# Optimization experiments

Measured on AMD Instinct MI355X. Metric: run time of the kernel, lower is better.

## Reference

```python
import jax, jax.numpy as jnp
import numpy as np

B, S, HID = 2, 2048, 1024
H, D = 16, HID // 16  # heads, head_dim
ROPE_BASE = 10000.0


def setup_inputs() -> dict:
    key = jax.random.key(0)
    k1, k2, k3, k4 = jax.random.split(key, 4)
    scale = 1.0 / np.sqrt(HID)
    return {
        "hidden_states": jax.random.normal(k1, (B, S, HID), dtype=jnp.float32),
        "attention_mask": jnp.zeros((B, 1, 1, S), dtype=jnp.float32),
        "Wq": jax.random.normal(k2, (HID, HID), dtype=jnp.float32) * scale,
        "Wk": jax.random.normal(k3, (HID, HID), dtype=jnp.float32) * scale,
        "Wv": jax.random.normal(k4, (HID, HID), dtype=jnp.float32) * scale,
    }


def _rope_cos_sin(seq_len, dim, dtype):
    inv_freq = 1.0 / (ROPE_BASE ** (jnp.arange(0, dim, 2, dtype=jnp.float32) / dim))
    freqs = jnp.arange(seq_len, dtype=jnp.float32)[:, None] * inv_freq[None, :]  # (S, D/2)
    emb = jnp.concatenate([freqs, freqs], axis=-1)  # (S, D)
    return jnp.cos(emb).astype(dtype), jnp.sin(emb).astype(dtype)


def _rotate_half(x):
    x1, x2 = jnp.split(x, 2, axis=-1)
    return jnp.concatenate([-x2, x1], axis=-1)


def reference(hidden_states, attention_mask, Wq, Wk, Wv):
    b, s, _ = hidden_states.shape
    # QKV projections (no bias), split into heads: (b, H, s, D)
    def proj(W):
        return jnp.einsum('bse,de->bsd', hidden_states, W).reshape(b, s, H, D).transpose(0, 2, 1, 3)
    q, k, v = proj(Wq), proj(Wk), proj(Wv)
    # Rotary embedding on q, k over sequence positions
    cos, sin = _rope_cos_sin(s, D, hidden_states.dtype)  # (s, D)
    cos = cos[None, None]  # (1,1,s,D)
    sin = sin[None, None]
    q = q * cos + _rotate_half(q) * sin
    k = k * cos + _rotate_half(k) * sin
    # Scaled dot-product attention with additive mask
    scores = jnp.einsum('bhqd,bhkd->bhqk', q, k) / jnp.sqrt(jnp.asarray(D, hidden_states.dtype))
    scores = scores + attention_mask
    probs = jax.nn.softmax(scores, axis=-1)  # dropout p=0 (eval) -> identity
    ctx = jnp.einsum('bhqk,bhkd->bhqd', probs, v)
    return ctx.transpose(0, 2, 1, 3).reshape(b, s, H * D)
```

## Files before the change

kernel.cpp:

```cpp
#include <hip/hip_runtime.h>
#include <stdint.h>

typedef unsigned short u16;
typedef short bf16x8 __attribute__((ext_vector_type(8)));
typedef float f32x4 __attribute__((ext_vector_type(4)));

#define S_ 2048
#define HID_ 1024
#define H_ 16
#define D_ 64

#define LOG2E 1.4426950408889634f
#define SCALE_LOG2 0.18033688011112042f
#define MAXC_LOG2 11.541560327111707f

__device__ __forceinline__ u16 f2bf(float f) {
  uint32_t x = __builtin_bit_cast(uint32_t, f);
  uint32_t r = (x + 0x7fffu + ((x >> 16) & 1u)) >> 16;
  return (u16)r;
}
__device__ __forceinline__ uint32_t packbf2(float a, float b) {
  return (uint32_t)f2bf(a) | ((uint32_t)f2bf(b) << 16);
}
__device__ __forceinline__ uint32_t permpack(float a, float b) {
  return __builtin_amdgcn_perm(__builtin_bit_cast(uint32_t, b),
                               __builtin_bit_cast(uint32_t, a), 0x07060302u);
}

__device__ __forceinline__ void gl2lds16(const void* g, void* l) {
  __builtin_amdgcn_global_load_lds(
      (const __attribute__((address_space(1))) unsigned int*)g,
      (__attribute__((address_space(3))) unsigned int*)l, 16, 0, 0);
}

#define NX_ (1 << 20)
#define NW_ (1 << 18)
#define NROPE_ 65536
__global__ void prep_kernel(const float* __restrict__ X, const float* __restrict__ Wq,
                            const float* __restrict__ Wk, const float* __restrict__ Wv,
                            const float* __restrict__ mask, u16* __restrict__ Xb,
                            u16* __restrict__ Wqb, u16* __restrict__ Wkb,
                            u16* __restrict__ Wvb, float* __restrict__ cos_t,
                            float* __restrict__ sin_t, float* __restrict__ mask2) {
  int i = blockIdx.x * 256 + threadIdx.x;
  if (i < NX_ + 3 * NW_) {
    const float* src;
    u16* dst;
    int off;
    if (i < NX_) {
      src = X; dst = Xb; off = i;
    } else if (i < NX_ + NW_) {
      src = Wq; dst = Wqb; off = i - NX_;
    } else if (i < NX_ + 2 * NW_) {
      src = Wk; dst = Wkb; off = i - NX_ - NW_;
    } else {
      src = Wv; dst = Wvb; off = i - NX_ - 2 * NW_;
    }
    float4 v = ((const float4*)src)[off];
    uint2 packed;
    packed.x = packbf2(v.x, v.y);
    packed.y = packbf2(v.z, v.w);
    ((uint2*)dst)[off] = packed;
  } else if (i < NX_ + 3 * NW_ + NROPE_) {
    int t = i - (NX_ + 3 * NW_);
    int s = t >> 5, j = t & 31;
    float invf = powf(10000.0f, -(float)j * (1.0f / 32.0f));
    float ang = (float)s * invf;
    cos_t[t] = cosf(ang);
    sin_t[t] = sinf(ang);
  } else {
    int t = i - (NX_ + 3 * NW_ + NROPE_);
    mask2[t] = fmaf(mask[t], LOG2E, -MAXC_LOG2);
  }
}

__global__ __launch_bounds__(512, 2) void qkv_gemm_kernel(
    const u16* __restrict__ X, const u16* __restrict__ Wq, const u16* __restrict__ Wk,
    const u16* __restrict__ Wv, const float* __restrict__ cos_t,
    const float* __restrict__ sin_t, u16* __restrict__ Q, u16* __restrict__ K,
    u16* __restrict__ Vt) {
  __shared__ char smem[131072];
  int tid = threadIdx.x;
  int lane = tid & 63, wave = tid >> 6;
  int wm = wave >> 2, wn = wave & 3;
  int quad = lane >> 4, l16 = lane & 15;
  int nbase = blockIdx.x * 128;
  int mbase = blockIdx.y * 128;

#define STAGE_ALL(k0, buf)                                                        \
  {                                                                               \
    _Pragma("unroll") for (int it = 0; it < 8; ++it) {                            \
      int j = (it & 1) * 512 + tid;                                               \
      int r = j >> 3, gs = j & 7, gsrc = gs ^ (r & 7);                            \
      const u16* src; int rb;                                                     \
      if ((it >> 1) == 0)      { src = X;  rb = mbase + r; }                      \
      else if ((it >> 1) == 1) { src = Wq; rb = nbase + r; }                      \
      else if ((it >> 1) == 2) { src = Wk; rb = nbase + r; }                      \
      else                     { src = Wv; rb = nbase + r; }                      \
      gl2lds16(src + (size_t)rb * HID_ + (k0) + gsrc * 8,                         \
               (buf) + (it >> 1) * 16384 + j * 16);                               \
    }                                                                             \
  }

  STAGE_ALL(0, smem)

  f32x4 acc[3][4][2] = {};

  for (int kk = 0; kk < 16; ++kk) {
    const char* buf = smem + (kk & 1) * 65536;
    __syncthreads();

    if (kk < 15)
      STAGE_ALL((kk + 1) * 64, smem + ((kk + 1) & 1) * 65536)

#pragma unroll
    for (int kh = 0; kh < 2; ++kh) {
      bf16x8 afrag[4];
#pragma unroll
      for (int i4 = 0; i4 < 4; ++i4) {
        int r = wm * 64 + i4 * 16 + l16;
        int L = r * 8 + ((kh * 4 + quad) ^ (r & 7));
        afrag[i4] = *(const bf16x8*)(buf + L * 16);
      }
#pragma unroll
      for (int w = 0; w < 3; ++w) {
        const char* Bs = buf + 16384 + w * 16384;
        bf16x8 bfrag[2];
#pragma unroll
        for (int j2 = 0; j2 < 2; ++j2) {
          int r = (wn >> 1) * 64 + (wn & 1) * 16 + j2 * 32 + l16;
          int L = r * 8 + ((kh * 4 + quad) ^ (r & 7));
          bfrag[j2] = *(const bf16x8*)(Bs + L * 16);
        }
        if (w == 2) {
#pragma unroll
          for (int i4 = 0; i4 < 4; ++i4)
#pragma unroll
            for (int j2 = 0; j2 < 2; ++j2)
              acc[2][i4][j2] = __builtin_amdgcn_mfma_f32_16x16x32_bf16(
                  afrag[i4], bfrag[j2], acc[2][i4][j2], 0, 0, 0);
        } else if (w == 1) {
#pragma unroll
          for (int i4 = 0; i4 < 4; ++i4)
#pragma unroll
            for (int j2 = 0; j2 < 2; ++j2)
              acc[1][i4][j2] = __builtin_amdgcn_mfma_f32_16x16x32_bf16(
                  bfrag[j2], afrag[i4], acc[1][i4][j2], 0, 0, 0);
        } else {
#pragma unroll
          for (int i4 = 0; i4 < 4; ++i4)
#pragma unroll
            for (int j2 = 0; j2 < 2; ++j2)
              acc[0][i4][j2] = __builtin_amdgcn_mfma_f32_16x16x32_bf16(
                  bfrag[j2], afrag[i4], acc[0][i4][j2], 0, 0, 0);
        }
      }
    }
  }
#undef STAGE_ALL

#pragma unroll
  for (int i4 = 0; i4 < 4; ++i4)
#pragma unroll
    for (int j2 = 0; j2 < 2; ++j2) {
      int m = mbase + wm * 64 + i4 * 16 + quad * 4;
      int n = nbase + (wn >> 1) * 64 + (wn & 1) * 16 + j2 * 32 + l16;
      int b = m >> 11, s0 = m & 2047;
      int h = n >> 6, d = n & 63;
      uint2 pk;
      pk.x = packbf2(acc[2][i4][j2][0], acc[2][i4][j2][1]);
      pk.y = packbf2(acc[2][i4][j2][2], acc[2][i4][j2][3]);
      *(uint2*)(Vt + (((size_t)(b * H_ + h)) * D_ + d) * S_ + s0) = pk;
    }

#pragma unroll
  for (int w = 0; w < 2; ++w) {
    u16* dst = (w == 0) ? Q : K;
#pragma unroll
    for (int i4 = 0; i4 < 4; ++i4) {
      int m = mbase + wm * 64 + i4 * 16 + l16;
      int n1 = nbase + (wn >> 1) * 64 + (wn & 1) * 16 + quad * 4;
      int b = m >> 11, s = m & 2047;
      int h = n1 >> 6, d1 = n1 & 63;
      float4 c4 = *(const float4*)(cos_t + s * 32 + d1);
      float4 s4 = *(const float4*)(sin_t + s * 32 + d1);
      float y1[4], y2[4];
#pragma unroll
      for (int r = 0; r < 4; ++r) {
        float cr = ((const float*)&c4)[r], sr = ((const float*)&s4)[r];
        float x1 = acc[w][i4][0][r], x2 = acc[w][i4][1][r];
        y1[r] = x1 * cr - x2 * sr;
        y2[r] = x2 * cr + x1 * sr;
      }
      size_t base = ((size_t)(b * H_ + h) * S_ + s) * D_;
      uint2 p1, p2;
      p1.x = packbf2(y1[0], y1[1]);
      p1.y = packbf2(y1[2], y1[3]);
      p2.x = packbf2(y2[0], y2[1]);
      p2.y = packbf2(y2[2], y2[3]);
      *(uint2*)(dst + base + d1) = p1;
      *(uint2*)(dst + base + d1 + 32) = p2;
    }
  }
}

__device__ __forceinline__ void pv_step(const bf16x8 (*pp)[2], const char* Vp, int quad,
                                        int l16, const bf16x8& ones, f32x4 (*o)[4],
                                        f32x4* lacc) {
  lacc[0] = __builtin_amdgcn_mfma_f32_16x16x32_bf16(pp[0][0], ones, lacc[0], 0, 0, 0);
  lacc[0] = __builtin_amdgcn_mfma_f32_16x16x32_bf16(pp[0][1], ones, lacc[0], 0, 0, 0);
  lacc[1] = __builtin_amdgcn_mfma_f32_16x16x32_bf16(pp[1][0], ones, lacc[1], 0, 0, 0);
  lacc[1] = __builtin_amdgcn_mfma_f32_16x16x32_bf16(pp[1][1], ones, lacc[1], 0, 0, 0);
#pragma unroll
  for (int jd = 0; jd < 4; ++jd) {
    int r = jd * 16 + l16;
#pragma unroll
    for (int kh = 0; kh < 2; ++kh) {
      int L = r * 8 + ((kh * 4 + quad) ^ (r & 7));
      bf16x8 vf = *(const bf16x8*)(Vp + L * 16);
      o[0][jd] = __builtin_amdgcn_mfma_f32_16x16x32_bf16(pp[0][kh], vf, o[0][jd], 0, 0, 0);
      o[1][jd] = __builtin_amdgcn_mfma_f32_16x16x32_bf16(pp[1][kh], vf, o[1][jd], 0, 0, 0);
    }
  }
}

__device__ __forceinline__ void qk_step(const char* Ks, const bf16x8 (*qfrag)[2], int quad,
                                        int l16, f32x4 (*s)[4]) {
#pragma unroll
  for (int jt = 0; jt < 4; ++jt) {
    int r = jt * 16 + l16;
#pragma unroll
    for (int kh = 0; kh < 2; ++kh) {
      int L = r * 8 + ((kh * 4 + quad) ^ (r & 7));
      bf16x8 kf = *(const bf16x8*)(Ks + L * 16);
      s[0][jt] = __builtin_amdgcn_mfma_f32_16x16x32_bf16(kf, qfrag[0][kh], s[0][jt], 0, 0, 0);
      s[1][jt] = __builtin_amdgcn_mfma_f32_16x16x32_bf16(kf, qfrag[1][kh], s[1][jt], 0, 0, 0);
    }
  }
}

__device__ __forceinline__ void softmax_pack(const f32x4 (*s)[4], const float4* mv,
                                             bf16x8 (*pp)[2]) {
#pragma unroll
  for (int qb = 0; qb < 2; ++qb) {
    uint32_t a[4][2];
#pragma unroll
    for (int jt = 0; jt < 4; ++jt) {
      float pf[4];
#pragma unroll
      for (int r = 0; r < 4; ++r) {
        float mvr = ((const float*)&mv[jt])[r];
        pf[r] = __builtin_amdgcn_exp2f(fmaf(s[qb][jt][r], SCALE_LOG2, mvr));
      }
      a[jt][0] = permpack(pf[0], pf[1]);
      a[jt][1] = permpack(pf[2], pf[3]);
    }
#pragma unroll
    for (int kh = 0; kh < 2; ++kh) {
      uint32_t tt[4];
#pragma unroll
      for (int i = 0; i < 2; ++i) {
        auto r1 = __builtin_amdgcn_permlane32_swap(a[2 * kh][i], a[2 * kh + 1][i],
                                                   false, false);
        auto r2 = __builtin_amdgcn_permlane16_swap(r1[0], r1[1], false, false);
        tt[i] = r2[0];
        tt[2 + i] = r2[1];
      }
      union { uint32_t u[4]; bf16x8 v; } cv;
      cv.u[0] = tt[0]; cv.u[1] = tt[1]; cv.u[2] = tt[2]; cv.u[3] = tt[3];
      pp[qb][kh] = cv.v;
    }
  }
}

__device__ __forceinline__ void stage_kv(const u16* Kbase, const u16* Vbase, char* Kn,
                                         int nb, int tid) {
#pragma unroll
  for (int half = 0; half < 2; ++half) {
    int i = half * 256 + tid;
    int r = i >> 3, gs = i & 7, gsrc = gs ^ (r & 7);
    gl2lds16(Kbase + (size_t)(nb + r) * D_ + gsrc * 8, Kn + i * 16);
    gl2lds16(Vbase + (size_t)r * S_ + nb + gsrc * 8, Kn + 8192 + i * 16);
  }
}

__global__ __launch_bounds__(256, 2) void flash_kernel(
    const u16* __restrict__ Q, const u16* __restrict__ K, const u16* __restrict__ Vt,
    const float* __restrict__ mask2, float* __restrict__ out) {
  __shared__ char smem[49152];
  int tid = threadIdx.x, wave = tid >> 6;
  int lane = tid & 63;
  int quad = lane >> 4, l16 = lane & 15;
  int bh = blockIdx.y, b = bh >> 4, h = bh & 15;
  int qbase = blockIdx.x * 128;
  int qw = qbase + wave * 32;
  const float* m2row = mask2 + b * S_;
  const u16* Kbase = K + (size_t)bh * S_ * D_;
  const u16* Vbase = Vt + (size_t)bh * D_ * S_;

  bf16x8 qfrag[2][2];
#pragma unroll
  for (int qb = 0; qb < 2; ++qb) {
    const u16* qp = Q + ((size_t)bh * S_ + qw + qb * 16 + l16) * D_ + quad * 8;
    qfrag[qb][0] = *(const bf16x8*)qp;
    qfrag[qb][1] = *(const bf16x8*)(qp + 32);
  }
  bf16x8 ones;
#pragma unroll
  for (int j = 0; j < 8; ++j) ones[j] = (short)0x3f80;

  f32x4 o[2][4] = {};
  f32x4 lacc[2] = {};
  bf16x8 pp[2][2];

  stage_kv(Kbase, Vbase, smem, 0, tid);
  float4 mv[4];
#pragma unroll
  for (int jt = 0; jt < 4; ++jt) mv[jt] = *(const float4*)(m2row + jt * 16 + quad * 4);

  {
    __syncthreads();
    stage_kv(Kbase, Vbase, smem + 16384, 64, tid);
    f32x4 s[2][4] = {};
    __builtin_amdgcn_s_setprio(1);
    qk_step(smem, qfrag, quad, l16, s);
    __builtin_amdgcn_s_setprio(0);
    softmax_pack(s, mv, pp);
#pragma unroll
    for (int jt = 0; jt < 4; ++jt)
      mv[jt] = *(const float4*)(m2row + 64 + jt * 16 + quad * 4);
  }

  for (int kt = 1; kt <= 30; ++kt) {
    char* Ks = smem + (kt % 3) * 16384;
    __syncthreads();
    stage_kv(Kbase, Vbase, smem + ((kt + 1) % 3) * 16384, (kt + 1) * 64, tid);

    __builtin_amdgcn_s_setprio(1);
    const char* Vp = smem + ((kt - 1) % 3) * 16384 + 8192;
    pv_step(pp, Vp, quad, l16, ones, o, lacc);

    f32x4 s[2][4] = {};
    qk_step(Ks, qfrag, quad, l16, s);
    __builtin_amdgcn_s_setprio(0);

    softmax_pack(s, mv, pp);
#pragma unroll
    for (int jt = 0; jt < 4; ++jt)
      mv[jt] = *(const float4*)(m2row + (kt + 1) * 64 + jt * 16 + quad * 4);
  }

  {
    __syncthreads();
    __builtin_amdgcn_s_setprio(1);
    pv_step(pp, smem + 0 * 16384 + 8192, quad, l16, ones, o, lacc);
    f32x4 s[2][4] = {};
    qk_step(smem + 16384, qfrag, quad, l16, s);
    __builtin_amdgcn_s_setprio(0);
    softmax_pack(s, mv, pp);
  }

  pv_step(pp, smem + 16384 + 8192, quad, l16, ones, o, lacc);

  float inv[2][4];
#pragma unroll
  for (int qb = 0; qb < 2; ++qb)
#pragma unroll
    for (int r = 0; r < 4; ++r) inv[qb][r] = 1.0f / lacc[qb][r];
#pragma unroll
  for (int qb = 0; qb < 2; ++qb)
#pragma unroll
    for (int jd = 0; jd < 4; ++jd) {
#pragma unroll
      for (int r = 0; r < 4; ++r) {
        int d = jd * 16 + l16;
        int q = qw + qb * 16 + quad * 4 + r;
        out[(((size_t)b * S_ + q) * H_ + h) * D_ + d] = o[qb][jd][r] * inv[qb][r];
      }
    }
}

extern "C" void kernel_launch(void* const* d_in, const int* in_sizes, int n_in,
                              void* d_out, int out_size, void* d_ws, size_t ws_size,
                              hipStream_t stream) {
  const float* hid = (const float*)d_in[0];
  const float* mask = (const float*)d_in[1];
  const float* Wq = (const float*)d_in[2];
  const float* Wk = (const float*)d_in[3];
  const float* Wv = (const float*)d_in[4];
  float* out = (float*)d_out;
  char* ws = (char*)d_ws;

  u16* Xbf = (u16*)ws;
  u16* Wqb = (u16*)(ws + (8u << 20));
  u16* Wkb = (u16*)(ws + (10u << 20));
  u16* Wvb = (u16*)(ws + (12u << 20));
  u16* Qb = (u16*)(ws + (14u << 20));
  u16* Kb = (u16*)(ws + (22u << 20));
  u16* Vtb = (u16*)(ws + (30u << 20));
  float* cos_t = (float*)(ws + (38u << 20));
  float* sin_t = (float*)(ws + (38u << 20) + (256u << 10));
  float* mask2 = (float*)(ws + (38u << 20) + (512u << 10));

  prep_kernel<<<7440, 256, 0, stream>>>(hid, Wq, Wk, Wv, mask, Xbf, Wqb, Wkb, Wvb,
                                        cos_t, sin_t, mask2);
  qkv_gemm_kernel<<<dim3(8, 32), 512, 0, stream>>>(Xbf, Wqb, Wkb, Wvb, cos_t, sin_t,
                                                   Qb, Kb, Vtb);
  flash_kernel<<<dim3(16, 32), 256, 0, stream>>>(Qb, Kb, Vtb, mask2, out);
}
```

Baseline: 160.2 us.

## Load K/V fragments directly from global into registers, dropping LDS staging

Removes the shared-memory triple-buffered K/V staging and its per-tile barriers. Each wave now loads its own K and V MFMA fragments straight from global memory into registers, prefetching the next tile after the current tile's MFMAs. This avoids LDS traffic and synchronisation, but each of the four waves re-reads the same K/V tile from global/L2 with no sharing across the block. It also leaves only about one stage of latency hiding.

```diff
diff --git a/kernel.cpp b/kernel.cpp
--- a/kernel.cpp
+++ b/kernel.cpp
@@ -204,41 +204,6 @@
   }
 }
 
-__device__ __forceinline__ void pv_step(const bf16x8 (*pp)[2], const char* Vp, int quad,
-                                        int l16, const bf16x8& ones, f32x4 (*o)[4],
-                                        f32x4* lacc) {
-  lacc[0] = __builtin_amdgcn_mfma_f32_16x16x32_bf16(pp[0][0], ones, lacc[0], 0, 0, 0);
-  lacc[0] = __builtin_amdgcn_mfma_f32_16x16x32_bf16(pp[0][1], ones, lacc[0], 0, 0, 0);
-  lacc[1] = __builtin_amdgcn_mfma_f32_16x16x32_bf16(pp[1][0], ones, lacc[1], 0, 0, 0);
-  lacc[1] = __builtin_amdgcn_mfma_f32_16x16x32_bf16(pp[1][1], ones, lacc[1], 0, 0, 0);
-#pragma unroll
-  for (int jd = 0; jd < 4; ++jd) {
-    int r = jd * 16 + l16;
-#pragma unroll
-    for (int kh = 0; kh < 2; ++kh) {
-      int L = r * 8 + ((kh * 4 + quad) ^ (r & 7));
-      bf16x8 vf = *(const bf16x8*)(Vp + L * 16);
-      o[0][jd] = __builtin_amdgcn_mfma_f32_16x16x32_bf16(pp[0][kh], vf, o[0][jd], 0, 0, 0);
-      o[1][jd] = __builtin_amdgcn_mfma_f32_16x16x32_bf16(pp[1][kh], vf, o[1][jd], 0, 0, 0);
-    }
-  }
-}
-
-__device__ __forceinline__ void qk_step(const char* Ks, const bf16x8 (*qfrag)[2], int quad,
-                                        int l16, f32x4 (*s)[4]) {
-#pragma unroll
-  for (int jt = 0; jt < 4; ++jt) {
-    int r = jt * 16 + l16;
-#pragma unroll
-    for (int kh = 0; kh < 2; ++kh) {
-      int L = r * 8 + ((kh * 4 + quad) ^ (r & 7));
-      bf16x8 kf = *(const bf16x8*)(Ks + L * 16);
-      s[0][jt] = __builtin_amdgcn_mfma_f32_16x16x32_bf16(kf, qfrag[0][kh], s[0][jt], 0, 0, 0);
-      s[1][jt] = __builtin_amdgcn_mfma_f32_16x16x32_bf16(kf, qfrag[1][kh], s[1][jt], 0, 0, 0);
-    }
-  }
-}
-
 __device__ __forceinline__ void softmax_pack(const f32x4 (*s)[4], const float4* mv,
                                              bf16x8 (*pp)[2]) {
 #pragma unroll
@@ -273,30 +238,17 @@
   }
 }
 
-__device__ __forceinline__ void stage_kv(const u16* Kbase, const u16* Vbase, char* Kn,
-                                         int nb, int tid) {
-#pragma unroll
-  for (int half = 0; half < 2; ++half) {
-    int i = half * 256 + tid;
-    int r = i >> 3, gs = i & 7, gsrc = gs ^ (r & 7);
-    gl2lds16(Kbase + (size_t)(nb + r) * D_ + gsrc * 8, Kn + i * 16);
-    gl2lds16(Vbase + (size_t)r * S_ + nb + gsrc * 8, Kn + 8192 + i * 16);
-  }
-}
-
 __global__ __launch_bounds__(256, 2) void flash_kernel(
     const u16* __restrict__ Q, const u16* __restrict__ K, const u16* __restrict__ Vt,
     const float* __restrict__ mask2, float* __restrict__ out) {
-  __shared__ char smem[49152];
   int tid = threadIdx.x, wave = tid >> 6;
   int lane = tid & 63;
   int quad = lane >> 4, l16 = lane & 15;
   int bh = blockIdx.y, b = bh >> 4, h = bh & 15;
-  int qbase = blockIdx.x * 128;
-  int qw = qbase + wave * 32;
+  int qw = blockIdx.x * 128 + wave * 32;
   const float* m2row = mask2 + b * S_;
-  const u16* Kbase = K + (size_t)bh * S_ * D_;
-  const u16* Vbase = Vt + (size_t)bh * D_ * S_;
+  const u16* kptr = K + (size_t)bh * S_ * D_ + (size_t)l16 * D_ + quad * 8;
+  const u16* vptr = Vt + (size_t)bh * D_ * S_ + (size_t)l16 * S_ + quad * 8;
 
   bf16x8 qfrag[2][2];
 #pragma unroll
@@ -311,56 +263,72 @@
 
   f32x4 o[2][4] = {};
   f32x4 lacc[2] = {};
-  bf16x8 pp[2][2];
-
-  stage_kv(Kbase, Vbase, smem, 0, tid);
+
+  bf16x8 kf[4][2], vf[4][2];
+#pragma unroll
+  for (int jt = 0; jt < 4; ++jt)
+#pragma unroll
+    for (int kh = 0; kh < 2; ++kh)
+      kf[jt][kh] = *(const bf16x8*)(kptr + (size_t)(jt * 16) * D_ + kh * 32);
+#pragma unroll
+  for (int jd = 0; jd < 4; ++jd)
+#pragma unroll
+    for (int kh = 0; kh < 2; ++kh)
+      vf[jd][kh] = *(const bf16x8*)(vptr + (size_t)(jd * 16) * S_ + kh * 32);
   float4 mv[4];
 #pragma unroll
   for (int jt = 0; jt < 4; ++jt) mv[jt] = *(const float4*)(m2row + jt * 16 + quad * 4);
 
-  {
-    __syncthreads();
-    stage_kv(Kbase, Vbase, smem + 16384, 64, tid);
+  for (int kt = 0; kt < 32; ++kt) {
+    int ktn = kt + (kt < 31);
+
     f32x4 s[2][4] = {};
     __builtin_amdgcn_s_setprio(1);
-    qk_step(smem, qfrag, quad, l16, s);
+#pragma unroll
+    for (int jt = 0; jt < 4; ++jt)
+#pragma unroll
+      for (int kh = 0; kh < 2; ++kh) {
+        s[0][jt] = __builtin_amdgcn_mfma_f32_16x16x32_bf16(kf[jt][kh], qfrag[0][kh],
+                                                           s[0][jt], 0, 0, 0);
+        s[1][jt] = __builtin_amdgcn_mfma_f32_16x16x32_bf16(kf[jt][kh], qfrag[1][kh],
+                                                           s[1][jt], 0, 0, 0);
+      }
     __builtin_amdgcn_s_setprio(0);
+
+#pragma unroll
+    for (int jt = 0; jt < 4; ++jt)
+#pragma unroll
+      for (int kh = 0; kh < 2; ++kh)
+        kf[jt][kh] = *(const bf16x8*)(kptr + ((size_t)ktn * 64 + jt * 16) * D_ + kh * 32);
+
+    bf16x8 pp[2][2];
     softmax_pack(s, mv, pp);
 #pragma unroll
     for (int jt = 0; jt < 4; ++jt)
-      mv[jt] = *(const float4*)(m2row + 64 + jt * 16 + quad * 4);
-  }
-
-  for (int kt = 1; kt <= 30; ++kt) {
-    char* Ks = smem + (kt % 3) * 16384;
-    __syncthreads();
-    stage_kv(Kbase, Vbase, smem + ((kt + 1) % 3) * 16384, (kt + 1) * 64, tid);
+      mv[jt] = *(const float4*)(m2row + ktn * 64 + jt * 16 + quad * 4);
 
     __builtin_amdgcn_s_setprio(1);
-    const char* Vp = smem + ((kt - 1) % 3) * 16384 + 8192;
-    pv_step(pp, Vp, quad, l16, ones, o, lacc);
-
-    f32x4 s[2][4] = {};
-    qk_step(Ks, qfrag, quad, l16, s);
+    lacc[0] = __builtin_amdgcn_mfma_f32_16x16x32_bf16(pp[0][0], ones, lacc[0], 0, 0, 0);
+    lacc[0] = __builtin_amdgcn_mfma_f32_16x16x32_bf16(pp[0][1], ones, lacc[0], 0, 0, 0);
+    lacc[1] = __builtin_amdgcn_mfma_f32_16x16x32_bf16(pp[1][0], ones, lacc[1], 0, 0, 0);
+    lacc[1] = __builtin_amdgcn_mfma_f32_16x16x32_bf16(pp[1][1], ones, lacc[1], 0, 0, 0);
+#pragma unroll
+    for (int jd = 0; jd < 4; ++jd)
+#pragma unroll
+      for (int kh = 0; kh < 2; ++kh) {
+        o[0][jd] = __builtin_amdgcn_mfma_f32_16x16x32_bf16(pp[0][kh], vf[jd][kh],
+                                                           o[0][jd], 0, 0, 0);
+        o[1][jd] = __builtin_amdgcn_mfma_f32_16x16x32_bf16(pp[1][kh], vf[jd][kh],
+                                                           o[1][jd], 0, 0, 0);
+      }
     __builtin_amdgcn_s_setprio(0);
 
-    softmax_pack(s, mv, pp);
-#pragma unroll
-    for (int jt = 0; jt < 4; ++jt)
-      mv[jt] = *(const float4*)(m2row + (kt + 1) * 64 + jt * 16 + quad * 4);
-  }
-
-  {
-    __syncthreads();
-    __builtin_amdgcn_s_setprio(1);
-    pv_step(pp, smem + 0 * 16384 + 8192, quad, l16, ones, o, lacc);
-    f32x4 s[2][4] = {};
-    qk_step(smem + 16384, qfrag, quad, l16, s);
-    __builtin_amdgcn_s_setprio(0);
-    softmax_pack(s, mv, pp);
-  }
-
-  pv_step(pp, smem + 16384 + 8192, quad, l16, ones, o, lacc);
+#pragma unroll
+    for (int jd = 0; jd < 4; ++jd)
+#pragma unroll
+      for (int kh = 0; kh < 2; ++kh)
+        vf[jd][kh] = *(const bf16x8*)(vptr + (size_t)(jd * 16) * S_ + ktn * 64 + kh * 32);
+  }
 
   float inv[2][4];
 #pragma unroll
```

Measured after the change: 236.6 us. +47.7%, slower.

## Deepen flash attention pipeline with separate K/V ring buffers and double score registers

Applied to the files above, without the earlier changes.

Restructures the attention main loop into a deeper software pipeline. K tiles now use a 2-slot ring and V tiles a 4-slot ring in LDS, and scores are held in two alternating register sets. In each iteration the loop issues PV for tile kt-2, QK for tile kt, and softmax for tile kt-1, so the exp/softmax work can overlap with the MFMA QK of the next tile. This costs more registers (an extra score set), which may pressure occupancy at 2 blocks/CU.

```diff
diff --git a/kernel.cpp b/kernel.cpp
--- a/kernel.cpp
+++ b/kernel.cpp
@@ -273,14 +273,14 @@
   }
 }
 
-__device__ __forceinline__ void stage_kv(const u16* Kbase, const u16* Vbase, char* Kn,
-                                         int nb, int tid) {
-#pragma unroll
-  for (int half = 0; half < 2; ++half) {
-    int i = half * 256 + tid;
+__device__ __forceinline__ void stage_kv2(const u16* Kbase, const u16* Vbase, char* Kd,
+                                          char* Vd, int nb, int tid) {
+#pragma unroll
+  for (int hh = 0; hh < 2; ++hh) {
+    int i = hh * 256 + tid;
     int r = i >> 3, gs = i & 7, gsrc = gs ^ (r & 7);
-    gl2lds16(Kbase + (size_t)(nb + r) * D_ + gsrc * 8, Kn + i * 16);
-    gl2lds16(Vbase + (size_t)r * S_ + nb + gsrc * 8, Kn + 8192 + i * 16);
+    gl2lds16(Kbase + (size_t)(nb + r) * D_ + gsrc * 8, Kd + i * 16);
+    gl2lds16(Vbase + (size_t)r * S_ + nb + gsrc * 8, Vd + i * 16);
   }
 }
 
@@ -292,8 +292,7 @@
   int lane = tid & 63;
   int quad = lane >> 4, l16 = lane & 15;
   int bh = blockIdx.y, b = bh >> 4, h = bh & 15;
-  int qbase = blockIdx.x * 128;
-  int qw = qbase + wave * 32;
+  int qw = blockIdx.x * 128 + wave * 32;
   const float* m2row = mask2 + b * S_;
   const u16* Kbase = K + (size_t)bh * S_ * D_;
   const u16* Vbase = Vt + (size_t)bh * D_ * S_;
@@ -311,56 +310,70 @@
 
   f32x4 o[2][4] = {};
   f32x4 lacc[2] = {};
+  f32x4 sA[2][4], sB[2][4];
   bf16x8 pp[2][2];
 
-  stage_kv(Kbase, Vbase, smem, 0, tid);
+#define ZERO_S(S)                                                 \
+  _Pragma("unroll") for (int qb = 0; qb < 2; ++qb)                \
+  _Pragma("unroll") for (int jt = 0; jt < 4; ++jt)                \
+      S[qb][jt] = (f32x4){0.f, 0.f, 0.f, 0.f};
+
+#define KSLOT(t) (smem + ((t) & 1) * 8192)
+#define VSLOT(t) (smem + 16384 + ((t) & 3) * 8192)
+
+  stage_kv2(Kbase, Vbase, KSLOT(0), VSLOT(0), 0, tid);
   float4 mv[4];
 #pragma unroll
   for (int jt = 0; jt < 4; ++jt) mv[jt] = *(const float4*)(m2row + jt * 16 + quad * 4);
 
-  {
-    __syncthreads();
-    stage_kv(Kbase, Vbase, smem + 16384, 64, tid);
-    f32x4 s[2][4] = {};
-    __builtin_amdgcn_s_setprio(1);
-    qk_step(smem, qfrag, quad, l16, s);
-    __builtin_amdgcn_s_setprio(0);
-    softmax_pack(s, mv, pp);
-#pragma unroll
-    for (int jt = 0; jt < 4; ++jt)
-      mv[jt] = *(const float4*)(m2row + 64 + jt * 16 + quad * 4);
-  }
-
-  for (int kt = 1; kt <= 30; ++kt) {
-    char* Ks = smem + (kt % 3) * 16384;
-    __syncthreads();
-    stage_kv(Kbase, Vbase, smem + ((kt + 1) % 3) * 16384, (kt + 1) * 64, tid);
-
-    __builtin_amdgcn_s_setprio(1);
-    const char* Vp = smem + ((kt - 1) % 3) * 16384 + 8192;
-    pv_step(pp, Vp, quad, l16, ones, o, lacc);
-
-    f32x4 s[2][4] = {};
-    qk_step(Ks, qfrag, quad, l16, s);
-    __builtin_amdgcn_s_setprio(0);
-
-    softmax_pack(s, mv, pp);
-#pragma unroll
-    for (int jt = 0; jt < 4; ++jt)
-      mv[jt] = *(const float4*)(m2row + (kt + 1) * 64 + jt * 16 + quad * 4);
-  }
-
-  {
-    __syncthreads();
-    __builtin_amdgcn_s_setprio(1);
-    pv_step(pp, smem + 0 * 16384 + 8192, quad, l16, ones, o, lacc);
-    f32x4 s[2][4] = {};
-    qk_step(smem + 16384, qfrag, quad, l16, s);
-    __builtin_amdgcn_s_setprio(0);
-    softmax_pack(s, mv, pp);
-  }
-
-  pv_step(pp, smem + 16384 + 8192, quad, l16, ones, o, lacc);
+  __syncthreads();
+  stage_kv2(Kbase, Vbase, KSLOT(1), VSLOT(1), 64, tid);
+  ZERO_S(sB)
+  __builtin_amdgcn_s_setprio(1);
+  qk_step(KSLOT(0), qfrag, quad, l16, sB);
+  __builtin_amdgcn_s_setprio(0);
+
+  __syncthreads();
+  stage_kv2(Kbase, Vbase, KSLOT(2), VSLOT(2), 128, tid);
+  ZERO_S(sA)
+  __builtin_amdgcn_s_setprio(1);
+  qk_step(KSLOT(1), qfrag, quad, l16, sA);
+  __builtin_amdgcn_s_setprio(0);
+  softmax_pack(sB, mv, pp);
+#pragma unroll
+  for (int jt = 0; jt < 4; ++jt)
+    mv[jt] = *(const float4*)(m2row + 64 + jt * 16 + quad * 4);
+
+#define FLASH_BODY(kt, CUR, PREV)                                                  \
+  {                                                                                \
+    __syncthreads();                                                               \
+    if ((kt) < 31)                                                                 \
+      stage_kv2(Kbase, Vbase, KSLOT((kt) + 1), VSLOT((kt) + 1), ((kt) + 1) * 64,   \
+                tid);                                                              \
+    __builtin_amdgcn_s_setprio(1);                                                 \
+    pv_step(pp, VSLOT((kt) - 2), quad, l16, ones, o, lacc);          \
+    ZERO_S(CUR)                                                                    \
+    qk_step(KSLOT(kt), qfrag, quad, l16, CUR);                          \
+    __builtin_amdgcn_s_setprio(0);                                                 \
+    softmax_pack(PREV, mv, pp);                                      \
+    _Pragma("unroll") for (int jt = 0; jt < 4; ++jt)                               \
+        mv[jt] = *(const float4*)(m2row + (kt) * 64 + jt * 16 + quad * 4);         \
+  }
+
+  for (int j = 0; j < 15; ++j) {
+    int kt0 = 2 * j + 2;
+    FLASH_BODY(kt0, sB, sA)
+    FLASH_BODY(kt0 + 1, sA, sB)
+  }
+#undef FLASH_BODY
+
+  pv_step(pp, VSLOT(30), quad, l16, ones, o, lacc);
+  softmax_pack(sA, mv, pp);
+  pv_step(pp, VSLOT(31), quad, l16, ones, o, lacc);
+
+#undef ZERO_S
+#undef KSLOT
+#undef VSLOT
 
   float inv[2][4];
 #pragma unroll
```

Result: no change. 159.2 us (-0.6%).
